# Performance work log

Measured on AMD Instinct MI355X. Metric: run time of the kernel, lower is better.

## Reference

```python
import jax, jax.numpy as jnp
import numpy as np

B, L, H, F, E = 32, 512, 768, 3072, 8  # sentences, seq_len, hidden, ffn, experts


def setup_inputs() -> dict:
    key = jax.random.key(0)
    kx, kl, k1, k2, k3, k4 = jax.random.split(key, 6)
    return {
        "hidden_states": jax.random.normal(kx, (B, L, H), dtype=jnp.float32),
        "router_labels": jax.random.randint(kl, (B,), 0, E, dtype=jnp.int32),
        "W1": jax.random.normal(k1, (E, H, F), dtype=jnp.float32) * 0.02,
        "b1": jnp.zeros((E, F), dtype=jnp.float32),
        "W2": jax.random.normal(k2, (E, F, H), dtype=jnp.float32) * 0.02,
        "b2": jnp.zeros((E, H), dtype=jnp.float32),
    }


def reference(hidden_states, router_labels, W1, b1, W2, b2):
    # Equivalent to: sort sentences by label, run each group through its
    # expert FFN, concat, unsort. Expressed as a gather of per-sentence
    # expert weights followed by batched GEMMs (same math, no data-dependent
    # shapes).
    W1g = W1[router_labels]            # [B, H, F]
    b1g = b1[router_labels][:, None]   # [B, 1, F]
    W2g = W2[router_labels]            # [B, F, H]
    b2g = b2[router_labels][:, None]   # [B, 1, H]
    h = jnp.einsum("blh,bhf->blf", hidden_states, W1g) + b1g
    h = jax.nn.gelu(h, approximate=False)
    out = jnp.einsum("blf,bfh->blh", h, W2g) + b2g
    return out
```

## Files before the change

kernel.cpp:

```cpp
#include <hip/hip_runtime.h>
#include <hip/hip_bf16.h>

#define NB   32
#define SEQ  512
#define HID  768
#define FFN  3072
#define NEXP 8

typedef float f32x4 __attribute__((ext_vector_type(4)));
typedef short s16x8 __attribute__((ext_vector_type(8)));

__device__ __forceinline__ unsigned short f2bf(float f) {
    return __builtin_bit_cast(unsigned short, (__bf16)f);
}

__device__ __forceinline__ float fast_exp2(float x) {
    float r; asm("v_exp_f32 %0, %1" : "=v"(r) : "v"(x)); return r;
}
__device__ __forceinline__ float fast_rcp(float x) {
    float r; asm("v_rcp_f32 %0, %1" : "=v"(r) : "v"(x)); return r;
}

__device__ __forceinline__ float gelu_fast(float v) {
    float u  = v * (0.7978845608f + 0.0356774081f * v * v);
    float t  = fast_exp2(-2.8853900817779268f * fabsf(u));
    float T  = (1.0f - t) * fast_rcp(1.0f + t);
    return 0.5f * v + 0.5f * fabsf(v) * T;
}

#define GLOAD16(gp, lp) __builtin_amdgcn_global_load_lds( \
    (const __attribute__((address_space(1))) unsigned int*)(gp), \
    (__attribute__((address_space(3))) unsigned int*)(lp), 16, 0, 0)

#define VMCNT(N) asm volatile("s_waitcnt vmcnt(%0)" :: "i"(N) : "memory")

__device__ __forceinline__ int get_xcc() {
    int x;
    asm volatile("s_getreg_b32 %0, hwreg(HW_REG_XCC_ID)" : "=s"(x));
    return x & 7;
}

__device__ __forceinline__ int claim_item(int* cnt, int myx, int Q) {
#pragma unroll 1
    for (int t = 0; t < 8; ++t) {
        int x = (myx + t) & 7;
        int s = atomicAdd(&cnt[x], 1);
        if (s < Q) return x * Q + s;
    }
    return -1;
}


__device__ __forceinline__ void cvt_w_body(
    const float* __restrict__ W, unsigned short* __restrict__ WP,
    unsigned short (*tile)[65], int nx, int ny, int bx, int by, int bz)
{
    const int C = nx * 64, R = ny * 64;
    const int cbg = bx * 64, rbg = by * 64;
    const float* src = W + (size_t)bz * R * C;
    const int x = threadIdx.x & 63, y0 = threadIdx.x >> 6;
#pragma unroll
    for (int i = 0; i < 16; i++) {
        int r = y0 + i * 4;
        tile[r][x] = f2bf(src[(size_t)(rbg + r) * C + cbg + x]);
    }
    __syncthreads();

    const int nt  = bx >> 2;
    const int NTn = nx >> 2;
    const int kt  = by;
    const int KT  = ny;
    char* out = (char*)WP + ((size_t)(bz * NTn + nt) * KT + kt) * 32768;

#pragma unroll
    for (int i = 0; i < 2; i++) {
        int cc  = threadIdx.x + i * 256;
        int n64 = cc >> 3, kc = cc & 7;
        int row = (bx & 3) * 64 + n64;
        int half = (row >> 5) & 1;
        int rr   = (row & 31) | (((row >> 6) & 3) << 5);
        int q    = (kc * 16) ^ ((row & 7) << 4);
        unsigned short o[8];
#pragma unroll
        for (int j = 0; j < 8; j++) o[j] = tile[kc * 8 + j][n64];
        *(s16x8*)(out + half * 16384 + rr * 128 + q) = *(s16x8*)o;
    }
}

__global__ __launch_bounds__(256) void prep_all(
    const float* __restrict__ X, const float* __restrict__ W1,
    const float* __restrict__ W2, const int* __restrict__ labels,
    unsigned short* __restrict__ XbP, unsigned short* __restrict__ W1P,
    unsigned short* __restrict__ W2P, int* __restrict__ perm)
{
    __shared__ unsigned short tile[64][65];
    const int bid = blockIdx.x;
    if (bid == 0) {
        int i = threadIdx.x;
        if (i < NB) {
            int li = labels[i];
            int rank = 0;
            for (int j = 0; j < NB; j++) {
                int lj = labels[j];
                if (lj < li || (lj == li && j < i)) rank++;
            }
            perm[rank] = i;
        }
        return;
    }
    if (bid <= 768) {
        const int b  = bid - 1;
        const int kt = b % 12;
        const int mt = (b / 12) & 1;
        const int bs = b / 24;
        const float* src = X + ((size_t)bs * SEQ + (size_t)mt * 256) * HID + kt * 64;
        char* out = (char*)XbP + (size_t)b * 32768;
#pragma unroll
        for (int i = 0; i < 8; i++) {
            int c = threadIdx.x + i * 256;
            int half = c >> 10;
            int rr   = (c >> 3) & 127;
            int c16  = c & 7;
            int row  = (rr & 63) + ((rr >> 6) << 7) + half * 64;
            int tb   = (c16 * 16) ^ ((row & 7) << 4);
            const float* sp = src + (size_t)row * HID + (tb >> 1);
            f32x4 a = *(const f32x4*)sp;
            f32x4 b4 = *(const f32x4*)(sp + 4);
            unsigned short o[8];
#pragma unroll
            for (int v = 0; v < 4; v++) o[v] = f2bf(a[v]);
#pragma unroll
            for (int v = 0; v < 4; v++) o[4 + v] = f2bf(b4[v]);
            *(s16x8*)(out + (size_t)c * 16) = *(s16x8*)o;
        }
        return;
    }
    if (bid <= 768 + 4608) {
        int idx = bid - 769;
        cvt_w_body(W1, W1P, tile, 48, 12, idx % 48, (idx / 48) % 12, idx / 576);
        return;
    }
    {
        int idx = bid - (769 + 4608);
        cvt_w_body(W2, W2P, tile, 12, 48, idx % 12, (idx / 12) % 48, idx / 576);
    }
}

template<bool ISA>
__device__ __forceinline__ void stage_lin(const char* tile, char* lds, int half, int tid)
{
#pragma unroll
    for (int p = 0; p < 2; p++) {
        int L  = p * 8192 + tid * 16;
        int rr = L >> 7;
        int cb = L & 127;
        int row = ISA ? ((rr & 63) + ((rr >> 6) << 7) + half * 64)
                      : ((rr & 31) + ((rr >> 5) << 6) + half * 32);
        GLOAD16(tile + half * 16384 + L, lds + (size_t)row * 128 + cb);
    }
}

__device__ __forceinline__ void read_af(const char* Ab, int arow_b, int k0, int ih, s16x8 (&a)[2][4])
{
    const int k1 = k0 ^ 64;
#pragma unroll
    for (int i = 0; i < 4; i++) {
        const char* p = Ab + arow_b + (ih * 64 + i * 16) * 128;
        a[0][i] = *(const s16x8*)(p + k0);
        a[1][i] = *(const s16x8*)(p + k1);
    }
}
__device__ __forceinline__ void read_bf(const char* Bb, int brow_b, int k0, int jh, s16x8 (&b)[2][2])
{
    const int k1 = k0 ^ 64;
#pragma unroll
    for (int j = 0; j < 2; j++) {
        const char* p = Bb + brow_b + (jh * 32 + j * 16) * 128;
        b[0][j] = *(const s16x8*)(p + k0);
        b[1][j] = *(const s16x8*)(p + k1);
    }
}

template<int IH, int JH>
__device__ __forceinline__ void mfma_quad(s16x8 (&a)[2][4], s16x8 (&b)[2][2], f32x4 (&acc)[8][4])
{
    __builtin_amdgcn_s_setprio(1);
#pragma unroll
    for (int kk = 0; kk < 2; kk++)
#pragma unroll
        for (int i = 0; i < 4; i++)
#pragma unroll
            for (int j = 0; j < 2; j++)
                acc[IH * 4 + i][JH * 2 + j] = __builtin_amdgcn_mfma_f32_16x16x32_bf16(
                    a[kk][i], b[kk][j], acc[IH * 4 + i][JH * 2 + j], 0, 0, 0);
    __builtin_amdgcn_s_setprio(0);
}

template<bool S1, bool S2, int VM>
__device__ __forceinline__ void gwindowT(
    const char* tA1, const char* tB1, const char* tA0, const char* tB0,
    char* Acur, char* Bcur, char* Anxt, char* Bnxt,
    int arow_b, int brow_b, int k0, int tid, f32x4 (&acc)[8][4])
{
    s16x8 a[2][4], b0[2][2], b1[2][2];
    read_af(Acur, arow_b, k0, 0, a);
    read_bf(Bcur, brow_b, k0, 0, b0);
    if constexpr (S1) stage_lin<true >(tA1, Anxt, 1, tid);
    __builtin_amdgcn_s_barrier();
    mfma_quad<0, 0>(a, b0, acc);
    __builtin_amdgcn_s_barrier();
    read_bf(Bcur, brow_b, k0, 1, b1);
    if constexpr (S1) stage_lin<false>(tB1, Bnxt, 1, tid);
    __builtin_amdgcn_s_barrier();
    mfma_quad<0, 1>(a, b1, acc);
    __builtin_amdgcn_s_barrier();
    read_af(Acur, arow_b, k0, 1, a);
    if constexpr (S2) stage_lin<true >(tA0, Acur, 0, tid);
    __builtin_amdgcn_s_barrier();
    mfma_quad<1, 1>(a, b1, acc);
    __builtin_amdgcn_s_barrier();
    if constexpr (S2) stage_lin<false>(tB0, Bcur, 0, tid);
    __builtin_amdgcn_s_barrier();
    mfma_quad<1, 0>(a, b0, acc);
    if constexpr (VM >= 0) VMCNT(VM);
    __builtin_amdgcn_s_barrier();
}

__device__ __forceinline__ void mainloopT(const char* At, const char* Bt, int KT,
    char* smem, int tid, int arow_b, int brow_b, int k0, f32x4 (&acc)[8][4])
{
    stage_lin<true >(At,          smem,          0, tid);
    stage_lin<false>(Bt,          smem + 65536,  0, tid);
    stage_lin<true >(At,          smem,          1, tid);
    stage_lin<false>(Bt,          smem + 65536,  1, tid);
    stage_lin<true >(At + 32768,  smem + 32768,  0, tid);
    stage_lin<false>(Bt + 32768,  smem + 98304,  0, tid);
    VMCNT(4);
    __builtin_amdgcn_s_barrier();

    int cur = 0;
    for (int kt = 0; kt < KT - 2; ++kt) {
        char* Ac = smem + (cur << 15);
        char* An = smem + ((cur ^ 1) << 15);
        char* Bc = smem + 65536 + (cur << 15);
        char* Bn = smem + 65536 + ((cur ^ 1) << 15);
        gwindowT<true, true, 4>(At + (size_t)(kt + 1) * 32768, Bt + (size_t)(kt + 1) * 32768,
                                At + (size_t)(kt + 2) * 32768, Bt + (size_t)(kt + 2) * 32768,
                                Ac, Bc, An, Bn, arow_b, brow_b, k0, tid, acc);
        cur ^= 1;
    }
    {
        char* Ac = smem + (cur << 15);
        char* An = smem + ((cur ^ 1) << 15);
        char* Bc = smem + 65536 + (cur << 15);
        char* Bn = smem + 65536 + ((cur ^ 1) << 15);
        gwindowT<true, false, 0>(At + (size_t)(KT - 1) * 32768, Bt + (size_t)(KT - 1) * 32768,
                                 nullptr, nullptr, Ac, Bc, An, Bn, arow_b, brow_b, k0, tid, acc);
        cur ^= 1;
    }
    {
        char* Ac = smem + (cur << 15);
        char* An = smem + ((cur ^ 1) << 15);
        char* Bc = smem + 65536 + (cur << 15);
        char* Bn = smem + 65536 + ((cur ^ 1) << 15);
        gwindowT<false, false, -1>(nullptr, nullptr, nullptr, nullptr,
                                   Ac, Bc, An, Bn, arow_b, brow_b, k0, tid, acc);
    }
}

__global__ __launch_bounds__(512, 2) void moe_gemm1(
    const unsigned short* __restrict__ XbP,
    const int*   __restrict__ labels,
    const int*   __restrict__ perm,
    const unsigned short* __restrict__ W1P,
    const float* __restrict__ B1,
    unsigned short* __restrict__ GP,
    int* __restrict__ cnt1)
{
    extern __shared__ char smem[];
    const int tid = threadIdx.x;
    const int myx = get_xcc();
    if (tid == 0) ((volatile int*)smem)[0] = claim_item(cnt1, myx, 96);
    __syncthreads();
    const int item = ((volatile int*)smem)[0];
    __syncthreads();
    if (item < 0) return;

    const int x    = item / 96;
    const int s    = item % 96;
    const int band = s >> 5;
    const int i    = s & 31;
    const int pair = i >> 2;
    const int c    = i & 3;
    const int bs = perm[x * 4 + (pair >> 1)];
    const int mt = pair & 1;
    const int nt = band * 4 + c;
    const int e  = labels[bs];

    const char* At = (const char*)XbP + (size_t)((bs * 2 + mt) * 12) * 32768;
    const char* Bt = (const char*)W1P + (size_t)((e * 12 + nt) * 12) * 32768;

    const int lane = tid & 63, w = tid >> 6;
    const int wm = (w >> 2) * 128, wn = (w & 3) * 64;
    const int fr = lane & 15, fq = lane >> 4;
    const int arow_b = (wm + fr) * 128, brow_b = (wn + fr) * 128;
    const int k0 = (fq * 16) ^ ((fr & 7) << 4);

    f32x4 acc[8][4];
#pragma unroll
    for (int i2 = 0; i2 < 8; i2++)
#pragma unroll
        for (int j = 0; j < 4; j++) acc[i2][j] = (f32x4)0.0f;

    mainloopT(At, Bt, 12, smem, tid, arow_b, brow_b, k0, acc);

    const float* b1g = B1 + (size_t)e * FFN + (size_t)nt * 256;
    float bias[4];
#pragma unroll
    for (int nj = 0; nj < 4; nj++) bias[nj] = b1g[wn + nj * 16 + fr];
#pragma unroll
    for (int mi = 0; mi < 8; mi++)
#pragma unroll
        for (int nj = 0; nj < 4; nj++) {
            const int col = wn + nj * 16 + fr;
#pragma unroll
            for (int r2 = 0; r2 < 4; r2++) {
                const int row = wm + mi * 16 + fq * 4 + r2;
                float v = acc[mi][nj][r2] + bias[nj];
                int byte = row * 512 + ((col * 2) ^ ((row & 7) << 4));
                *(unsigned short*)(smem + byte) = f2bf(gelu_fast(v));
            }
        }
    __syncthreads();
    char* GPb = (char*)GP + ((size_t)(bs * 2 + mt) * 48 + (size_t)nt * 4) * 32768;
#pragma unroll
    for (int it = 0; it < 16; it++) {
        int c2 = tid + it * 512;
        int kt2l = c2 >> 11;
        int reg  = (c2 >> 10) & 1;
        int rr2  = (c2 >> 3) & 127;
        int c16  = c2 & 7;
        int row  = (rr2 & 63) + ((rr2 >> 6) << 7) + reg * 64;
        s16x8 v = *(const s16x8*)(smem + row * 512 + kt2l * 128 + c16 * 16);
        __builtin_nontemporal_store(v,
            (s16x8*)(GPb + (size_t)kt2l * 32768 + (size_t)(c2 & 2047) * 16));
    }
}

__global__ __launch_bounds__(512, 2) void moe_gemm2(
    const unsigned short* __restrict__ GP,
    const int*   __restrict__ labels,
    const int*   __restrict__ perm,
    const unsigned short* __restrict__ W2P,
    const float* __restrict__ B2,
    float* __restrict__ Out,
    int* __restrict__ cnt2)
{
    extern __shared__ char smem[];
    const int tid = threadIdx.x;
    const int myx = get_xcc();
    if (tid == 0) ((volatile int*)smem)[0] = claim_item(cnt2, myx, 24);
    __syncthreads();
    const int item = ((volatile int*)smem)[0];
    __syncthreads();
    if (item < 0) return;

    const int x = item / 24;
    const int s = item % 24;
    const int bs = perm[x * 4 + s / 6];
    const int rr = s % 6;
    const int mt = rr / 3, nt = rr % 3;
    const int e  = labels[bs];

    const char* At = (const char*)GP  + (size_t)((bs * 2 + mt) * 48) * 32768;
    const char* Bt = (const char*)W2P + (size_t)((e * 3 + nt) * 48) * 32768;

    const int lane = tid & 63, w = tid >> 6;
    const int wm = (w >> 2) * 128, wn = (w & 3) * 64;
    const int fr = lane & 15, fq = lane >> 4;
    const int arow_b = (wm + fr) * 128, brow_b = (wn + fr) * 128;
    const int k0 = (fq * 16) ^ ((fr & 7) << 4);

    f32x4 acc[8][4];
#pragma unroll
    for (int i = 0; i < 8; i++)
#pragma unroll
        for (int j = 0; j < 4; j++) acc[i][j] = (f32x4)0.0f;

    mainloopT(At, Bt, 48, smem, tid, arow_b, brow_b, k0, acc);

    const float* b2g = B2 + (size_t)e * HID + (size_t)nt * 256;
    float bias[4];
#pragma unroll
    for (int nj = 0; nj < 4; nj++) bias[nj] = b2g[wn + nj * 16 + fr];
    char* Cgb = (char*)(Out + ((size_t)bs * SEQ + (size_t)mt * 256) * HID + (size_t)nt * 256);

#pragma unroll
    for (int half = 0; half < 2; ++half) {
        if ((wn >> 7) == half) {
#pragma unroll
            for (int mi = 0; mi < 8; mi++)
#pragma unroll
                for (int nj = 0; nj < 4; nj++) {
                    const int lcol = (wn & 127) + nj * 16 + fr;
#pragma unroll
                    for (int r2 = 0; r2 < 4; r2++) {
                        const int row = wm + mi * 16 + fq * 4 + r2;
                        int byte = row * 512 + ((lcol * 4) ^ ((row & 7) << 4));
                        *(float*)(smem + byte) = acc[mi][nj][r2] + bias[nj];
                    }
                }
        }
        __syncthreads();
#pragma unroll
        for (int it = 0; it < 16; it++) {
            int chunk = tid + it * 512;
            int row = chunk >> 5;
            int cb  = (chunk & 31) * 16;
            f32x4 v = *(const f32x4*)(smem + row * 512 + (cb ^ ((row & 7) << 4)));
            __builtin_nontemporal_store(v, (f32x4*)(Cgb + (size_t)row * (HID * 4) + half * 512 + cb));
        }
        if (half == 0) __syncthreads();
    }
}

extern "C" void kernel_launch(void* const* d_in, const int* in_sizes, int n_in,
                              void* d_out, int out_size, void* d_ws, size_t ws_size,
                              hipStream_t stream) {
    const float* X      = (const float*)d_in[0];
    const int*   labels = (const int*)  d_in[1];
    const float* W1     = (const float*)d_in[2];
    const float* B1     = (const float*)d_in[3];
    const float* W2     = (const float*)d_in[4];
    const float* B2     = (const float*)d_in[5];
    float* Out = (float*)d_out;

    char* ws = (char*)d_ws;
    unsigned short* XbP = (unsigned short*)(ws);
    unsigned short* W1P = (unsigned short*)(ws + 25165824);
    unsigned short* W2P = (unsigned short*)(ws + 62914560);
    unsigned short* GP  = (unsigned short*)(ws + 100663296);
    int*            perm = (int*)(ws + 201326592);
    int*            cnt1 = (int*)(ws + 201326720);
    int*            cnt2 = (int*)(ws + 201326752);

    (void)hipFuncSetAttribute((const void*)moe_gemm1,
        hipFuncAttributeMaxDynamicSharedMemorySize, 131072);
    (void)hipFuncSetAttribute((const void*)moe_gemm2,
        hipFuncAttributeMaxDynamicSharedMemorySize, 131072);

    (void)hipMemsetAsync(cnt1, 0, 64, stream);

    prep_all<<<1 + 768 + 4608 + 4608, 256, 0, stream>>>(
        X, W1, W2, labels, XbP, W1P, W2P, perm);

    moe_gemm1<<<768, dim3(512), 131072, stream>>>(XbP, labels, perm, W1P, B1, GP, cnt1);
    moe_gemm2<<<192, dim3(512), 131072, stream>>>(GP, labels, perm, W2P, B2, Out, cnt2);
}
```

Before: 234.4 us.

## Load W1 fragments directly from global into registers in GEMM1

Rewrites the GEMM1 main loop so the B operand (expert W1 tiles) is read straight from global memory into registers using precomputed per-lane offsets, double-buffered in two register sets. Only the A operand is staged through shared memory, which cuts LDS traffic and the number of barriers per K step. The cost is more vector registers held live per thread and exposed global-load latency if prefetch depth is not enough, with a risk of spills at the two-blocks-per-CU launch bound.

```diff
diff --git a/kernel.cpp b/kernel.cpp
--- a/kernel.cpp
+++ b/kernel.cpp
@@ -196,6 +196,164 @@
     __builtin_amdgcn_s_setprio(0);
 }
 
+__device__ __forceinline__ void load_b8(const char* bt, const int* boff, s16x8 (&b)[8])
+{
+#pragma unroll
+    for (int i = 0; i < 8; i++)
+        b[i] = *(const s16x8*)(bt + boff[i]);
+}
+
+template<int IH>
+__device__ __forceinline__ void mfma_half(s16x8 (&a)[2][4], s16x8 (&b)[8], f32x4 (&acc)[8][4])
+{
+    __builtin_amdgcn_s_setprio(1);
+#pragma unroll
+    for (int kk = 0; kk < 2; kk++)
+#pragma unroll
+        for (int i = 0; i < 4; i++)
+#pragma unroll
+            for (int jh = 0; jh < 2; jh++)
+#pragma unroll
+                for (int j = 0; j < 2; j++)
+                    acc[IH * 4 + i][jh * 2 + j] = __builtin_amdgcn_mfma_f32_16x16x32_bf16(
+                        a[kk][i], b[jh * 4 + j * 2 + kk], acc[IH * 4 + i][jh * 2 + j], 0, 0, 0);
+    __builtin_amdgcn_s_setprio(0);
+}
+
+template<bool STG, int VM>
+__device__ __forceinline__ void bwin(const char* At2, const char* Bt2,
+    char* bufc, const int* boff, int arow_b, int k0, int tid,
+    s16x8 (&bC)[8], f32x4 (&acc)[8][4])
+{
+    s16x8 a[2][4];
+    read_af(bufc, arow_b, k0, 0, a);
+    mfma_half<0>(a, bC, acc);
+    read_af(bufc, arow_b, k0, 1, a);
+    asm volatile("s_waitcnt lgkmcnt(0)" ::: "memory");
+    __builtin_amdgcn_s_barrier();
+    if constexpr (STG) {
+        stage_lin<true>(At2, bufc, 0, tid);
+        stage_lin<true>(At2, bufc, 1, tid);
+    }
+    mfma_half<1>(a, bC, acc);
+    if constexpr (STG) load_b8(Bt2, boff, bC);
+    if constexpr (VM >= 0) VMCNT(VM);
+    __builtin_amdgcn_s_barrier();
+}
+
+__global__ __launch_bounds__(512, 2) void moe_gemm1(
+    const unsigned short* __restrict__ XbP,
+    const int*   __restrict__ labels,
+    const int*   __restrict__ perm,
+    const unsigned short* __restrict__ W1P,
+    const float* __restrict__ B1,
+    unsigned short* __restrict__ GP,
+    int* __restrict__ cnt1)
+{
+    extern __shared__ char smem[];
+    const int tid = threadIdx.x;
+    const int myx = get_xcc();
+    if (tid == 0) ((volatile int*)smem)[0] = claim_item(cnt1, myx, 96);
+    __syncthreads();
+    const int item = ((volatile int*)smem)[0];
+    __syncthreads();
+    if (item < 0) return;
+
+    const int x    = item / 96;
+    const int s    = item % 96;
+    const int band = s >> 5;
+    const int i    = s & 31;
+    const int pair = i >> 2;
+    const int c    = i & 3;
+    const int bs = perm[x * 4 + (pair >> 1)];
+    const int mt = pair & 1;
+    const int nt = band * 4 + c;
+    const int e  = labels[bs];
+
+    const char* At = (const char*)XbP + (size_t)((bs * 2 + mt) * 12) * 32768;
+    const char* Bt = (const char*)W1P + (size_t)((e * 12 + nt) * 12) * 32768;
+
+    const int lane = tid & 63, w = tid >> 6;
+    const int wm = (w >> 2) * 128, wn = (w & 3) * 64;
+    const int fr = lane & 15, fq = lane >> 4;
+    const int arow_b = (wm + fr) * 128;
+    const int k0 = (fq * 16) ^ ((fr & 7) << 4);
+
+    int boff[8];
+#pragma unroll
+    for (int jh = 0; jh < 2; jh++)
+#pragma unroll
+        for (int j = 0; j < 2; j++) {
+            int row  = wn + jh * 32 + j * 16 + fr;
+            int base = ((row >> 5) & 1) * 16384 +
+                       (((row & 31) | (((row >> 6) & 3) << 5))) * 128;
+#pragma unroll
+            for (int kk = 0; kk < 2; kk++)
+                boff[jh * 4 + j * 2 + kk] = base + ((kk * 64 + fq * 16) ^ ((row & 7) << 4));
+        }
+
+    f32x4 acc[8][4];
+#pragma unroll
+    for (int i2 = 0; i2 < 8; i2++)
+#pragma unroll
+        for (int j = 0; j < 4; j++) acc[i2][j] = (f32x4)0.0f;
+
+    s16x8 bE[8], bO[8];
+    stage_lin<true>(At,          smem,          0, tid);
+    stage_lin<true>(At,          smem,          1, tid);
+    stage_lin<true>(At + 32768,  smem + 32768,  0, tid);
+    stage_lin<true>(At + 32768,  smem + 32768,  1, tid);
+    load_b8(Bt,          boff, bE);
+    load_b8(Bt + 32768,  boff, bO);
+    VMCNT(20);
+    __builtin_amdgcn_s_barrier();
+
+#pragma unroll 1
+    for (int ww = 0; ww < 10; ww += 2) {
+        bwin<true, 20>(At + (size_t)(ww + 2) * 32768, Bt + (size_t)(ww + 2) * 32768,
+                       smem,         boff, arow_b, k0, tid, bE, acc);
+        bwin<true, 20>(At + (size_t)(ww + 3) * 32768, Bt + (size_t)(ww + 3) * 32768,
+                       smem + 32768, boff, arow_b, k0, tid, bO, acc);
+    }
+    bwin<false, 8>(nullptr, nullptr, smem,         boff, arow_b, k0, tid, bE, acc);
+    bwin<false, -1>(nullptr, nullptr, smem + 32768, boff, arow_b, k0, tid, bO, acc);
+
+    asm volatile("s_waitcnt lgkmcnt(0)" ::: "memory");
+    __syncthreads();
+
+    const float* b1g = B1 + (size_t)e * FFN + (size_t)nt * 256;
+    float bias[4];
+#pragma unroll
+    for (int nj = 0; nj < 4; nj++) bias[nj] = b1g[wn + nj * 16 + fr];
+#pragma unroll
+    for (int mi = 0; mi < 8; mi++)
+#pragma unroll
+        for (int nj = 0; nj < 4; nj++) {
+            const int col = wn + nj * 16 + fr;
+#pragma unroll
+            for (int r2 = 0; r2 < 4; r2++) {
+                const int row = wm + mi * 16 + fq * 4 + r2;
+                float v = acc[mi][nj][r2] + bias[nj];
+                int byte = row * 512 + ((col * 2) ^ ((row & 7) << 4));
+                *(unsigned short*)(smem + byte) = f2bf(gelu_fast(v));
+            }
+        }
+    __syncthreads();
+    char* GPb = (char*)GP + ((size_t)(bs * 2 + mt) * 48 + (size_t)nt * 4) * 32768;
+#pragma unroll
+    for (int it = 0; it < 16; it++) {
+        int c2 = tid + it * 512;
+        int kt2l = c2 >> 11;
+        int reg  = (c2 >> 10) & 1;
+        int rr2  = (c2 >> 3) & 127;
+        int c16  = c2 & 7;
+        int row  = (rr2 & 63) + ((rr2 >> 6) << 7) + reg * 64;
+        s16x8 v = *(const s16x8*)(smem + row * 512 + kt2l * 128 + c16 * 16);
+        __builtin_nontemporal_store(v,
+            (s16x8*)(GPb + (size_t)kt2l * 32768 + (size_t)(c2 & 2047) * 16));
+    }
+}
+
 template<bool S1, bool S2, int VM>
 __device__ __forceinline__ void gwindowT(
     const char* tA1, const char* tB1, const char* tA0, const char* tB0,
@@ -268,85 +426,6 @@
     }
 }
 
-__global__ __launch_bounds__(512, 2) void moe_gemm1(
-    const unsigned short* __restrict__ XbP,
-    const int*   __restrict__ labels,
-    const int*   __restrict__ perm,
-    const unsigned short* __restrict__ W1P,
-    const float* __restrict__ B1,
-    unsigned short* __restrict__ GP,
-    int* __restrict__ cnt1)
-{
-    extern __shared__ char smem[];
-    const int tid = threadIdx.x;
-    const int myx = get_xcc();
-    if (tid == 0) ((volatile int*)smem)[0] = claim_item(cnt1, myx, 96);
-    __syncthreads();
-    const int item = ((volatile int*)smem)[0];
-    __syncthreads();
-    if (item < 0) return;
-
-    const int x    = item / 96;
-    const int s    = item % 96;
-    const int band = s >> 5;
-    const int i    = s & 31;
-    const int pair = i >> 2;
-    const int c    = i & 3;
-    const int bs = perm[x * 4 + (pair >> 1)];
-    const int mt = pair & 1;
-    const int nt = band * 4 + c;
-    const int e  = labels[bs];
-
-    const char* At = (const char*)XbP + (size_t)((bs * 2 + mt) * 12) * 32768;
-    const char* Bt = (const char*)W1P + (size_t)((e * 12 + nt) * 12) * 32768;
-
-    const int lane = tid & 63, w = tid >> 6;
-    const int wm = (w >> 2) * 128, wn = (w & 3) * 64;
-    const int fr = lane & 15, fq = lane >> 4;
-    const int arow_b = (wm + fr) * 128, brow_b = (wn + fr) * 128;
-    const int k0 = (fq * 16) ^ ((fr & 7) << 4);
-
-    f32x4 acc[8][4];
-#pragma unroll
-    for (int i2 = 0; i2 < 8; i2++)
-#pragma unroll
-        for (int j = 0; j < 4; j++) acc[i2][j] = (f32x4)0.0f;
-
-    mainloopT(At, Bt, 12, smem, tid, arow_b, brow_b, k0, acc);
-
-    const float* b1g = B1 + (size_t)e * FFN + (size_t)nt * 256;
-    float bias[4];
-#pragma unroll
-    for (int nj = 0; nj < 4; nj++) bias[nj] = b1g[wn + nj * 16 + fr];
-#pragma unroll
-    for (int mi = 0; mi < 8; mi++)
-#pragma unroll
-        for (int nj = 0; nj < 4; nj++) {
-            const int col = wn + nj * 16 + fr;
-#pragma unroll
-            for (int r2 = 0; r2 < 4; r2++) {
-                const int row = wm + mi * 16 + fq * 4 + r2;
-                float v = acc[mi][nj][r2] + bias[nj];
-                int byte = row * 512 + ((col * 2) ^ ((row & 7) << 4));
-                *(unsigned short*)(smem + byte) = f2bf(gelu_fast(v));
-            }
-        }
-    __syncthreads();
-    char* GPb = (char*)GP + ((size_t)(bs * 2 + mt) * 48 + (size_t)nt * 4) * 32768;
-#pragma unroll
-    for (int it = 0; it < 16; it++) {
-        int c2 = tid + it * 512;
-        int kt2l = c2 >> 11;
-        int reg  = (c2 >> 10) & 1;
-        int rr2  = (c2 >> 3) & 127;
-        int c16  = c2 & 7;
-        int row  = (rr2 & 63) + ((rr2 >> 6) << 7) + reg * 64;
-        s16x8 v = *(const s16x8*)(smem + row * 512 + kt2l * 128 + c16 * 16);
-        __builtin_nontemporal_store(v,
-            (s16x8*)(GPb + (size_t)kt2l * 32768 + (size_t)(c2 & 2047) * 16));
-    }
-}
-
 __global__ __launch_bounds__(512, 2) void moe_gemm2(
     const unsigned short* __restrict__ GP,
     const int*   __restrict__ labels,
```

Result: slower. 260.3 us (+11.1%).
